# Kernel optimization log

Measured on AMD Instinct MI355X. Metric: run time of the kernel, lower is better.

The kernel has to match this reference:

```python
import jax, jax.numpy as jnp
import numpy as np

N = 100000   # nodes
E = 1600000  # edges (avg degree 16)
F = 64       # input feature dim
H = 64       # hidden dim
O = 64       # conv output dim
C = 2        # channels (x.shape[1])
S = 1000     # number of subgraphs
M = 64       # nodes per subgraph
MH = 128     # MLP hidden
OUT = 1      # MLP output


def setup_inputs() -> dict:
    key = jax.random.key(0)
    ks = jax.random.split(key, 16)
    x = jax.random.normal(ks[0], (N, C, F), jnp.float32)
    edge_index = jax.random.randint(ks[1], (2, E), 0, N, dtype=jnp.int32)
    edge_weight = jax.random.uniform(ks[2], (E,), jnp.float32)
    subG_node = jax.random.randint(ks[3], (S, M), 0, N, dtype=jnp.int32)
    s1 = 1.0 / np.sqrt(F)
    s2 = 1.0 / np.sqrt(H)
    sm1 = 1.0 / np.sqrt(O)
    sm2 = 1.0 / np.sqrt(MH)
    return {
        "x": x,
        "edge_index": edge_index,
        "edge_weight": edge_weight,
        "subG_node": subG_node,
        "W1": jax.random.normal(ks[4], (F, H), jnp.float32) * s1,
        "b1": jnp.zeros((H,), jnp.float32),
        "gn_w": jnp.ones((H,), jnp.float32),
        "gn_b": jnp.zeros((H,), jnp.float32),
        "gn_ms": jnp.ones((H,), jnp.float32),
        "W2": jax.random.normal(ks[5], (H, O), jnp.float32) * s2,
        "b2": jnp.zeros((O,), jnp.float32),
        "mW1": jax.random.normal(ks[6], (O, MH), jnp.float32) * sm1,
        "mb1": jnp.zeros((MH,), jnp.float32),
        "mW2": jax.random.normal(ks[7], (MH, OUT), jnp.float32) * sm2,
        "mb2": jnp.zeros((OUT,), jnp.float32),
    }


def _graph_norm(h, w, b, ms, eps=1e-5):
    # PyG GraphNorm over all nodes (single graph): per-feature stats
    mean = jnp.mean(h, axis=0, keepdims=True)
    out = h - ms * mean
    var = jnp.mean(out * out, axis=0, keepdims=True)
    return w * out * jax.lax.rsqrt(var + eps) + b


def _gcn_layer(h, src, dst, norm, self_norm, W, b, n):
    # GCNConv: h' = D^-1/2 (A + I) D^-1/2 (h @ W) + b
    hw = h @ W                                   # [N, out]
    msg = norm[:, None] * hw[src]                # [E, out] gather
    agg = jax.ops.segment_sum(msg, dst, num_segments=n)  # scatter-add
    agg = agg + self_norm[:, None] * hw          # self-loop term
    return agg + b


def reference(x, edge_index, edge_weight, subG_node,
              W1, b1, gn_w, gn_b, gn_ms, W2, b2, mW1, mb1, mW2, mb2):
    n = x.shape[0]
    src, dst = edge_index[0], edge_index[1]
    # symmetric GCN normalization with self-loops of weight 1
    deg = jax.ops.segment_sum(edge_weight, dst, num_segments=n) + 1.0
    dinv = jax.lax.rsqrt(deg)
    norm = dinv[src] * edge_weight * dinv[dst]   # [E]
    self_norm = dinv * dinv                      # [N]

    def conv_channel(xc):  # xc: [N, F]
        h = _gcn_layer(xc, src, dst, norm, self_norm, W1, b1, n)
        h = _graph_norm(h, gn_w, gn_b, gn_ms)
        h = jax.nn.relu(h)
        return _gcn_layer(h, src, dst, norm, self_norm, W2, b2, n)

    emb = jax.vmap(conv_channel, in_axes=1, out_axes=1)(x)  # [N, C, O]
    emb = jnp.mean(emb, axis=1)                              # [N, O]
    # subgraph pooling: sp @ emb == sum of member-node embeddings
    pooled = jnp.sum(emb[subG_node], axis=1)                 # [S, O]
    h = jax.nn.relu(pooled @ mW1 + mb1)
    return h @ mW2 + mb2                                     # [S, 1]
```

## Files before the change

kernel.cpp:

```cpp
#include <hip/hip_runtime.h>
#include <hip/hip_fp16.h>


#define NNODES 100000
#define NEDGES 1600000
#define NSUB   1000

#define WSHIFT 9
#define WIN    512
#define NWIN   196
#define WCAP   10240
#define NBLK   256
#define CHUNK  (NEDGES / NBLK)

typedef _Float16 f16x8 __attribute__((ext_vector_type(8)));
typedef float    f32x4 __attribute__((ext_vector_type(4)));


__global__ __launch_bounds__(256) void k_bin(const int* __restrict__ src,
                                             const int* __restrict__ dst,
                                             const float* __restrict__ ew,
                                             int* __restrict__ wcur,
                                             int2* __restrict__ esw,
                                             const int* __restrict__ subg,
                                             int* __restrict__ flags) {
    __shared__ int hist[NWIN];
    __shared__ int base[NWIN];
    __shared__ int fill[NWIN];
    int t = threadIdx.x, b = blockIdx.x;
    if (t < 250) flags[subg[b * 250 + t]] = 1;
    for (int i = t; i < NWIN; i += 256) { hist[i] = 0; fill[i] = 0; }
    __syncthreads();
    int e0 = b * CHUNK;
    for (int e = e0 + t; e < e0 + CHUNK; e += 256)
        atomicAdd(&hist[dst[e] >> WSHIFT], 1);
    __syncthreads();
    for (int i = t; i < NWIN; i += 256) {
        int c = hist[i];
        base[i] = c ? atomicAdd(&wcur[i], c) : 0;
    }
    __syncthreads();
    for (int e = e0 + t; e < e0 + CHUNK; e += 256) {
        int d = dst[e];
        int w = d >> WSHIFT;
        int pos = base[w] + atomicAdd(&fill[w], 1);
        if (pos < WCAP) {
            int dl = d - (w << WSHIFT);
            esw[(size_t)w * WCAP + pos] =
                make_int2((dl << 17) | src[e], __float_as_int(ew[e]));
        }
    }
}

__global__ __launch_bounds__(256) void k_fill2(const int* __restrict__ wcur,
                                               const int2* __restrict__ esw,
                                               unsigned* __restrict__ edges,
                                               int* __restrict__ row_ptr,
                                               int* __restrict__ cnt,
                                               float* __restrict__ dinv) {
    __shared__ int   cnt_l[WIN];
    __shared__ int   sc[WIN];
    __shared__ int   fill_l[WIN];
    __shared__ float degw[WIN];
    int t = threadIdx.x, w = blockIdx.x;
    #pragma unroll
    for (int i = t; i < WIN; i += 256) { cnt_l[i] = 0; fill_l[i] = 0; degw[i] = 0.f; }
    __syncthreads();
    int e0 = w * WCAP;
    int count = wcur[w]; if (count > WCAP) count = WCAP;
    int e1 = e0 + count;
    for (int e = e0 + t; e < e1; e += 256) {
        int2 v = esw[e];
        int dl = ((unsigned)v.x) >> 17;
        atomicAdd(&cnt_l[dl], 1);
        atomicAdd(&degw[dl], __int_as_float(v.y));
    }
    __syncthreads();
    sc[t] = cnt_l[t]; sc[t + 256] = cnt_l[t + 256];
    __syncthreads();
    for (int off = 1; off < WIN; off <<= 1) {
        int v0 = (t >= off) ? sc[t - off] : 0;
        int v1 = (t + 256 >= off) ? sc[t + 256 - off] : 0;
        __syncthreads();
        sc[t] += v0; sc[t + 256] += v1;
        __syncthreads();
    }
    sc[t]       = e0 + sc[t]       - cnt_l[t];
    sc[t + 256] = e0 + sc[t + 256] - cnt_l[t + 256];
    __syncthreads();
    for (int e = e0 + t; e < e1; e += 256) {
        int2 v = esw[e];
        int dl = ((unsigned)v.x) >> 17;
        int pos = sc[dl] + atomicAdd(&fill_l[dl], 1);
        int wq = __float2int_rn(__int_as_float(v.y) * 32767.0f);
        edges[pos] = ((unsigned)wq << 17) | ((unsigned)v.x & 0x1FFFFu);
    }
    __syncthreads();
    #pragma unroll
    for (int i = t; i < WIN; i += 256) {
        int node = (w << WSHIFT) + i;
        if (node < NNODES) {
            row_ptr[node] = sc[i];
            cnt[node]     = cnt_l[i];
            dinv[node]    = rsqrtf(degw[i] + 1.0f);
        }
    }
}


template <bool TR>
__global__ __launch_bounds__(256) void k_gemm(const void* __restrict__ Xv,
                                              const float* __restrict__ Wg,
                                              const float* __restrict__ dinv,
                                              _Float16* __restrict__ Y,
                                              const float* __restrict__ partial,
                                              const float* __restrict__ gn_w,
                                              const float* __restrict__ gn_b,
                                              const float* __restrict__ gn_ms) {
    __shared__ __align__(16) _Float16 ob[4][16 * 72];
    __shared__ float st[256];
    int t = threadIdx.x;
    int wave = t >> 6, lane = t & 63;
    int m = lane & 15, q = lane >> 4;

    if constexpr (TR) {
        float s = 0.f;
        #pragma unroll 4
        for (int j = 0; j < 64; j++) s += partial[j * 256 + t];
        st[t] = s;
    }

    f16x8 bf[2][4];
    #pragma unroll
    for (int kb = 0; kb < 2; kb++)
        #pragma unroll
        for (int nt = 0; nt < 4; nt++)
            #pragma unroll
            for (int j = 0; j < 8; j++)
                bf[kb][nt][j] = (_Float16)Wg[(kb * 32 + q * 8 + j) * 64 + nt * 16 + m];

    float ca[16], cb[16];
    if constexpr (TR) {
        __syncthreads();
        int c = m & 1;
        const float inv_n = 1.0f / (float)NNODES;
        #pragma unroll
        for (int kb = 0; kb < 2; kb++)
            #pragma unroll
            for (int j = 0; j < 8; j++) {
                int k = kb * 32 + q * 8 + j;
                int col = c * 64 + k;
                float mean = st[col] * inv_n;
                float eh2  = st[128 + col] * inv_n;
                float ms   = gn_ms[k];
                float mm   = ms * mean;
                float var  = eh2 - 2.0f * mm * mean + mm * mm;
                float A = gn_w[k] * rsqrtf(var + 1e-5f);
                ca[kb * 8 + j] = A;
                cb[kb * 8 + j] = gn_b[k] - A * mm;
            }
    }

    int tile = blockIdx.x * 4 + wave;
    int row0 = tile * 16;

    f16x8 af[2];
    if constexpr (!TR) {
        const float* xp = (const float*)Xv + (size_t)(row0 + m) * 64;
        #pragma unroll
        for (int kb = 0; kb < 2; kb++) {
            float4 u0 = *(const float4*)(xp + kb * 32 + q * 8);
            float4 u1 = *(const float4*)(xp + kb * 32 + q * 8 + 4);
            af[kb][0] = (_Float16)u0.x; af[kb][1] = (_Float16)u0.y;
            af[kb][2] = (_Float16)u0.z; af[kb][3] = (_Float16)u0.w;
            af[kb][4] = (_Float16)u1.x; af[kb][5] = (_Float16)u1.y;
            af[kb][6] = (_Float16)u1.z; af[kb][7] = (_Float16)u1.w;
        }
    } else {
        const _Float16* xp = (const _Float16*)Xv + (size_t)(row0 + m) * 64;
        #pragma unroll
        for (int kb = 0; kb < 2; kb++) {
            f16x8 v = *(const f16x8*)(xp + kb * 32 + q * 8);
            #pragma unroll
            for (int j = 0; j < 8; j++) {
                float f = (float)v[j];
                f = fmaxf(ca[kb * 8 + j] * f + cb[kb * 8 + j], 0.0f);
                af[kb][j] = (_Float16)f;
            }
        }
    }

    f32x4 acc[4];
    #pragma unroll
    for (int nt = 0; nt < 4; nt++) {
        acc[nt] = (f32x4){0.f, 0.f, 0.f, 0.f};
        acc[nt] = __builtin_amdgcn_mfma_f32_16x16x32_f16(af[0], bf[0][nt], acc[nt], 0, 0, 0);
        acc[nt] = __builtin_amdgcn_mfma_f32_16x16x32_f16(af[1], bf[1][nt], acc[nt], 0, 0, 0);
    }

    float dv[4];
    #pragma unroll
    for (int i = 0; i < 4; i++) dv[i] = dinv[(row0 + q * 4 + i) >> 1];

    _Float16* obw = ob[wave];
    #pragma unroll
    for (int nt = 0; nt < 4; nt++)
        #pragma unroll
        for (int i = 0; i < 4; i++)
            obw[(q * 4 + i) * 72 + nt * 16 + m] = (_Float16)(acc[nt][i] * dv[i]);
    __syncthreads();

    _Float16* yp = Y + (size_t)row0 * 64;
    #pragma unroll
    for (int s = 0; s < 2; s++) {
        int c8 = s * 64 + lane;
        int r = c8 >> 3, cg2 = c8 & 7;
        uint4 v = *(const uint4*)(obw + r * 72 + cg2 * 8);
        *(uint4*)(yp + (size_t)r * 64 + cg2 * 8) = v;
    }
}


template <bool USE_FLAGS, bool STATS>
__global__ __launch_bounds__(256) void k_prop(const __half* __restrict__ hw,
                                              const float* __restrict__ bias,
                                              const float* __restrict__ dinv,
                                              const int* __restrict__ row_ptr,
                                              const int* __restrict__ cnt,
                                              const unsigned* __restrict__ edges,
                                              const int* __restrict__ flags,
                                              __half* __restrict__ agg,
                                              float* __restrict__ partial) {
    __shared__ float ssum[128];
    __shared__ float ssq[128];
    int t = threadIdx.x;
    int lane = t & 63;
    int n = __builtin_amdgcn_readfirstlane(blockIdx.x * 4 + (t >> 6));

    if constexpr (STATS) {
        if (t < 128) ssum[t] = 0.f; else ssq[t - 128] = 0.f;
        __syncthreads();
    }
    if constexpr (USE_FLAGS) { if (flags[n] != 1) return; }

    int f = lane * 2;
    int feat = f & 63;
    const float qs = 1.0f / 32767.0f;

    float2 bv = *(const float2*)(bias + feat);
    float dv = dinv[n];
    float2 self = __half22float2(*(const __half2*)(hw + (size_t)n * 128 + f));
    float acc0 = self.x;
    float acc1 = self.y;

    int start = row_ptr[n];
    int cn    = cnt[n];
    const unsigned* pp = edges + start;

    int full = cn & ~15;
    int p = 0;
    for (; p < full; p += 16) {
        unsigned e[16];
        #pragma unroll
        for (int i = 0; i < 16; i++) e[i] = pp[p + i];
        float2 h[16];
        #pragma unroll
        for (int i = 0; i < 16; i++) {
            int s = (int)(e[i] & 0x1FFFFu);
            h[i] = __half22float2(*(const __half2*)(hw + (size_t)s * 128 + f));
        }
        #pragma unroll
        for (int i = 0; i < 16; i++) {
            float w = (float)(e[i] >> 17) * qs;
            acc0 += w * h[i].x;
            acc1 += w * h[i].y;
        }
    }
    if (p < cn) {
        unsigned e[16];
        #pragma unroll
        for (int i = 0; i < 16; i++) e[i] = pp[p + i];
        float2 h[16];
        #pragma unroll
        for (int i = 0; i < 16; i++) {
            int s = (int)(e[i] & 0x1FFFFu);
            h[i] = __half22float2(*(const __half2*)(hw + (size_t)s * 128 + f));
        }
        #pragma unroll
        for (int i = 0; i < 16; i++) {
            float w = ((p + i) < cn) ? (float)(e[i] >> 17) * qs : 0.0f;
            acc0 += w * h[i].x;
            acc1 += w * h[i].y;
        }
    }

    float r0 = dv * acc0 + bv.x;
    float r1 = dv * acc1 + bv.y;
    *(__half2*)(agg + (size_t)n * 128 + f) = __floats2half2_rn(r0, r1);

    if constexpr (STATS) {
        atomicAdd(&ssum[f], r0);     atomicAdd(&ssum[f + 1], r1);
        atomicAdd(&ssq[f], r0 * r0); atomicAdd(&ssq[f + 1], r1 * r1);
        __syncthreads();
        float v = (t < 128) ? ssum[t] : ssq[t - 128];
        atomicAdd(&partial[(blockIdx.x & 63) * 256 + t], v);
    }
}


__global__ __launch_bounds__(256) void k_head(const __half* __restrict__ agg,
                                              const int* __restrict__ subg,
                                              const float* __restrict__ mW1,
                                              const float* __restrict__ mb1,
                                              const float* __restrict__ mW2,
                                              const float* __restrict__ mb2,
                                              float* __restrict__ out) {
    __shared__ int   idx[64];
    __shared__ float pl[4][64];
    __shared__ float red[128];
    int s = blockIdx.x, t = threadIdx.x;
    if (t < 64) idx[t] = subg[s * 64 + t];
    __syncthreads();
    int j = t & 63, grp = t >> 6;
    float acc = 0.f;
    #pragma unroll
    for (int m = grp * 16; m < grp * 16 + 16; m++) {
        int n = idx[m];
        acc += __half2float(agg[(size_t)n * 128 + j]) +
               __half2float(agg[(size_t)n * 128 + 64 + j]);
    }
    pl[grp][j] = acc * 0.5f;
    __syncthreads();
    if (t < 64) pl[0][t] = pl[0][t] + pl[1][t] + pl[2][t] + pl[3][t];
    __syncthreads();
    if (t < 128) {
        float h = mb1[t];
        #pragma unroll
        for (int k = 0; k < 64; k++) h += pl[0][k] * mW1[k * 128 + t];
        h = fmaxf(h, 0.0f);
        red[t] = h * mW2[t];
    }
    __syncthreads();
    for (int off = 64; off > 0; off >>= 1) {
        if (t < off) red[t] += red[t + off];
        __syncthreads();
    }
    if (t == 0) out[s] = red[0] + mb2[0];
}


extern "C" void kernel_launch(void* const* d_in, const int* in_sizes, int n_in,
                              void* d_out, int out_size, void* d_ws, size_t ws_size,
                              hipStream_t stream) {
    const float* x     = (const float*)d_in[0];
    const int*   ei    = (const int*)d_in[1];
    const float* ew    = (const float*)d_in[2];
    const int*   subg  = (const int*)d_in[3];
    const float* W1    = (const float*)d_in[4];
    const float* b1    = (const float*)d_in[5];
    const float* gn_w  = (const float*)d_in[6];
    const float* gn_b  = (const float*)d_in[7];
    const float* gn_ms = (const float*)d_in[8];
    const float* W2    = (const float*)d_in[9];
    const float* b2    = (const float*)d_in[10];
    const float* mW1   = (const float*)d_in[11];
    const float* mb1   = (const float*)d_in[12];
    const float* mW2   = (const float*)d_in[13];
    const float* mb2   = (const float*)d_in[14];
    float* out = (float*)d_out;

    char* w = (char*)d_ws;
    size_t off = 0;
    auto alloc = [&](size_t bytes) {
        void* p = w + off;
        off = (off + bytes + 255) & ~(size_t)255;
        return p;
    };
    int*      wcur    = (int*)     alloc(NWIN * 4);
    float*    partial = (float*)   alloc(64 * 256 * 4);
    float*    dinv    = (float*)   alloc((size_t)NNODES * 4);
    int*      cnt     = (int*)     alloc((size_t)NNODES * 4);
    int*      row_ptr = (int*)     alloc((size_t)NNODES * 4);
    int*      flags   = (int*)     alloc((size_t)NNODES * 4);
    unsigned* edges   = (unsigned*)alloc(((size_t)NWIN * WCAP + 64) * 4);
    int2*     esw     = (int2*)    alloc((size_t)NWIN * WCAP * 8);
    __half*   hw      = (__half*)  alloc((size_t)NNODES * 128 * 2);
    __half*   agg     = (__half*)  alloc((size_t)NNODES * 128 * 2);

    const int* src = ei;
    const int* dst = ei + NEDGES;

    size_t zspan = (size_t)((char*)(partial + 64 * 256) - (char*)wcur);
    hipMemsetAsync(wcur, 0, zspan, stream);

    k_bin  <<<NBLK, 256, 0, stream>>>(src, dst, ew, wcur, esw, subg, flags);
    k_fill2<<<NWIN, 256, 0, stream>>>(wcur, esw, edges, row_ptr, cnt, dinv);

    k_gemm<false><<<3125, 256, 0, stream>>>(x, W1, dinv, (_Float16*)hw,
                                            nullptr, nullptr, nullptr, nullptr);
    k_prop<false, true><<<25000, 256, 0, stream>>>(hw, b1, dinv, row_ptr, cnt, edges,
                                                   nullptr, agg, partial);

    k_gemm<true><<<3125, 256, 0, stream>>>(agg, W2, dinv, (_Float16*)hw,
                                           partial, gn_w, gn_b, gn_ms);
    k_prop<true, false><<<25000, 256, 0, stream>>>(hw, b2, dinv, row_ptr, cnt, edges,
                                                   flags, agg, nullptr);

    k_head<<<NSUB, 256, 0, stream>>>(agg, subg, mW1, mb1, mW2, mb2, out);
}
```

Measured before the change: 409.5 us.

## Move GraphNorm statistics out of propagation into a separate reduction kernel

```diff
diff --git a/kernel.cpp b/kernel.cpp
--- a/kernel.cpp
+++ b/kernel.cpp
@@ -113,22 +113,14 @@
                                               const float* __restrict__ Wg,
                                               const float* __restrict__ dinv,
                                               _Float16* __restrict__ Y,
-                                              const float* __restrict__ partial,
+                                              const float* __restrict__ stats,
                                               const float* __restrict__ gn_w,
                                               const float* __restrict__ gn_b,
                                               const float* __restrict__ gn_ms) {
     __shared__ __align__(16) _Float16 ob[4][16 * 72];
-    __shared__ float st[256];
     int t = threadIdx.x;
     int wave = t >> 6, lane = t & 63;
     int m = lane & 15, q = lane >> 4;
-
-    if constexpr (TR) {
-        float s = 0.f;
-        #pragma unroll 4
-        for (int j = 0; j < 64; j++) s += partial[j * 256 + t];
-        st[t] = s;
-    }
 
     f16x8 bf[2][4];
     #pragma unroll
@@ -141,7 +133,6 @@
 
     float ca[16], cb[16];
     if constexpr (TR) {
-        __syncthreads();
         int c = m & 1;
         const float inv_n = 1.0f / (float)NNODES;
         #pragma unroll
@@ -150,8 +141,8 @@
             for (int j = 0; j < 8; j++) {
                 int k = kb * 32 + q * 8 + j;
                 int col = c * 64 + k;
-                float mean = st[col] * inv_n;
-                float eh2  = st[128 + col] * inv_n;
+                float mean = stats[col] * inv_n;
+                float eh2  = stats[128 + col] * inv_n;
                 float ms   = gn_ms[k];
                 float mm   = ms * mean;
                 float var  = eh2 - 2.0f * mm * mean + mm * mm;
@@ -221,7 +212,7 @@
 }
 
 
-template <bool USE_FLAGS, bool STATS>
+template <bool USE_FLAGS>
 __global__ __launch_bounds__(256) void k_prop(const __half* __restrict__ hw,
                                               const float* __restrict__ bias,
                                               const float* __restrict__ dinv,
@@ -229,18 +220,10 @@
                                               const int* __restrict__ cnt,
                                               const unsigned* __restrict__ edges,
                                               const int* __restrict__ flags,
-                                              __half* __restrict__ agg,
-                                              float* __restrict__ partial) {
-    __shared__ float ssum[128];
-    __shared__ float ssq[128];
+                                              __half* __restrict__ agg) {
     int t = threadIdx.x;
     int lane = t & 63;
     int n = __builtin_amdgcn_readfirstlane(blockIdx.x * 4 + (t >> 6));
-
-    if constexpr (STATS) {
-        if (t < 128) ssum[t] = 0.f; else ssq[t - 128] = 0.f;
-        __syncthreads();
-    }
     if constexpr (USE_FLAGS) { if (flags[n] != 1) return; }
 
     int f = lane * 2;
@@ -294,16 +277,40 @@
         }
     }
 
-    float r0 = dv * acc0 + bv.x;
-    float r1 = dv * acc1 + bv.y;
-    *(__half2*)(agg + (size_t)n * 128 + f) = __floats2half2_rn(r0, r1);
-
-    if constexpr (STATS) {
-        atomicAdd(&ssum[f], r0);     atomicAdd(&ssum[f + 1], r1);
-        atomicAdd(&ssq[f], r0 * r0); atomicAdd(&ssq[f + 1], r1 * r1);
-        __syncthreads();
-        float v = (t < 128) ? ssum[t] : ssq[t - 128];
-        atomicAdd(&partial[(blockIdx.x & 63) * 256 + t], v);
+    *(__half2*)(agg + (size_t)n * 128 + f) =
+        __floats2half2_rn(dv * acc0 + bv.x, dv * acc1 + bv.y);
+}
+
+
+__global__ __launch_bounds__(256) void k_stats(const __half* __restrict__ agg,
+                                               float* __restrict__ stats) {
+    __shared__ float ls[16][128];
+    __shared__ float lq[16][128];
+    int t = threadIdx.x;
+    int cb = (t & 15) * 8;
+    int rg = t >> 4;
+    float s[8], q[8];
+    #pragma unroll
+    for (int i = 0; i < 8; i++) { s[i] = 0.f; q[i] = 0.f; }
+    for (int r = blockIdx.x * 16 + rg; r < NNODES; r += gridDim.x * 16) {
+        uint4 u = *(const uint4*)(agg + (size_t)r * 128 + cb);
+        const __half2* h2 = (const __half2*)&u;
+        #pragma unroll
+        for (int i = 0; i < 4; i++) {
+            float2 v = __half22float2(h2[i]);
+            s[2*i]   += v.x; q[2*i]   += v.x * v.x;
+            s[2*i+1] += v.y; q[2*i+1] += v.y * v.y;
+        }
+    }
+    #pragma unroll
+    for (int i = 0; i < 8; i++) { ls[rg][cb + i] = s[i]; lq[rg][cb + i] = q[i]; }
+    __syncthreads();
+    if (t < 128) {
+        float a = 0.f, b = 0.f;
+        #pragma unroll
+        for (int g = 0; g < 16; g++) { a += ls[g][t]; b += lq[g][t]; }
+        atomicAdd(&stats[t], a);
+        atomicAdd(&stats[128 + t], b);
     }
 }
 
@@ -377,7 +384,7 @@
         return p;
     };
     int*      wcur    = (int*)     alloc(NWIN * 4);
-    float*    partial = (float*)   alloc(64 * 256 * 4);
+    float*    stats   = (float*)   alloc(512 * 4);
     float*    dinv    = (float*)   alloc((size_t)NNODES * 4);
     int*      cnt     = (int*)     alloc((size_t)NNODES * 4);
     int*      row_ptr = (int*)     alloc((size_t)NNODES * 4);
@@ -390,7 +397,7 @@
     const int* src = ei;
     const int* dst = ei + NEDGES;
 
-    size_t zspan = (size_t)((char*)(partial + 64 * 256) - (char*)wcur);
+    size_t zspan = (size_t)((char*)(stats + 512) - (char*)wcur);
     hipMemsetAsync(wcur, 0, zspan, stream);
 
     k_bin  <<<NBLK, 256, 0, stream>>>(src, dst, ew, wcur, esw, subg, flags);
@@ -398,13 +405,15 @@
 
     k_gemm<false><<<3125, 256, 0, stream>>>(x, W1, dinv, (_Float16*)hw,
                                             nullptr, nullptr, nullptr, nullptr);
-    k_prop<false, true><<<25000, 256, 0, stream>>>(hw, b1, dinv, row_ptr, cnt, edges,
-                                                   nullptr, agg, partial);
+    k_prop<false><<<25000, 256, 0, stream>>>(hw, b1, dinv, row_ptr, cnt, edges,
+                                             nullptr, agg);
+
+    k_stats<<<512, 256, 0, stream>>>(agg, stats);
 
     k_gemm<true><<<3125, 256, 0, stream>>>(agg, W2, dinv, (_Float16*)hw,
-                                           partial, gn_w, gn_b, gn_ms);
-    k_prop<true, false><<<25000, 256, 0, stream>>>(hw, b2, dinv, row_ptr, cnt, edges,
-                                                   flags, agg, nullptr);
+                                           stats, gn_w, gn_b, gn_ms);
+    k_prop<true><<<25000, 256, 0, stream>>>(hw, b2, dinv, row_ptr, cnt, edges,
+                                            flags, agg);
 
     k_head<<<NSUB, 256, 0, stream>>>(agg, subg, mW1, mb1, mW2, mb2, out);
 }
```

Result: faster. 329.5 us (-19.5%).
